# Optimization experiments

Hardware: AMD Instinct MI355X
Metric: run time of the kernel (lower is better)

Reference implementation:

```python
import jax, jax.numpy as jnp
from jax import lax
import numpy as np

EPS = 1e-3  # epsilon from __init__


def setup_inputs() -> dict:
    key = jax.random.key(0)
    k_x, k_m, k_v, k_p = jax.random.split(key, 4)
    B, C, H, W = 16, 64, 128, 128
    K = 8  # num_contexts
    x = jax.random.normal(k_x, (B, C, H, W), dtype=jnp.float32)
    # Parameters as initialized by reset_parameters():
    mean = jax.random.uniform(k_m, (K, 1), minval=-1.0, maxval=1.0, dtype=jnp.float32)
    variance = jax.random.uniform(k_v, (K, 1), minval=0.001, maxval=0.01, dtype=jnp.float32)
    p0 = jax.random.uniform(k_p, (K, 1), dtype=jnp.float32)
    prior = p0 / jnp.sum(p0, axis=0, keepdims=True)
    return {"x": x, "mean": mean, "variance": variance, "prior": prior}


def reference(x, mean, variance, prior):
    # Eval-mode forward of AdaptiveContextNorm (4D input path).
    mu = mean[:, 0]                      # (K,) scalar mean per context (expand over C is a broadcast)
    v = jax.nn.softplus(variance[:, 0])  # (K,)
    pr = jax.nn.softmax(prior[:, 0], axis=0)  # (K,)

    # Pass 1: mixture denominator. NOTE: faithful to source, the denominator
    # uses var WITHOUT +eps in the 4D path (ternary-precedence quirk), while
    # the numerator p_x_given_k uses (var + eps).
    def denom_step(acc, params):
        m, vv, pk = params
        return acc + pk * jnp.exp(-0.5 * ((x - m) / vv) ** 2), None

    denom, _ = lax.scan(denom_step, jnp.zeros_like(x), (mu, v, pr))

    # Pass 2: accumulate normalized output.
    def out_step(acc, params):
        m, vv, pk = params
        p_x_given_k = pk * jnp.exp(-0.5 * ((x - m) / (vv + EPS)) ** 2)
        tau_k = p_x_given_k / (denom + EPS)
        hat_x = (x - m) / jnp.sqrt(vv + EPS)
        return acc + tau_k / jnp.sqrt(pk + EPS) * hat_x, None

    out, _ = lax.scan(out_step, jnp.zeros_like(x), (mu, v, pr))
    return out
```

## Files before the change

kernel.cpp:

```cpp
#include <hip/hip_runtime.h>
#include <hip/hip_fp16.h>

#define ACN_EPS   0.001f
#define ACN_LOG2E 1.4426950408889634f
#define ACN_LN2   0.6931471805599453f
#define TBL_N     2048
#define TBL_LO    -8.0f
#define TBL_SCALE 128.0f
#define TBL_OFF   1024.0f
#define TBL_MAX_T 2047.999f

typedef float v4f  __attribute__((ext_vector_type(4)));
typedef unsigned int u32;
typedef u32 v4u __attribute__((ext_vector_type(4)));

__device__ __forceinline__ float acn_F_fast(float x, const float* mu,
                                            const float* s1, const float* lp,
                                            const float* s2, const float* lw) {
    float denom = 0.0f, S = 0.0f;
#pragma unroll
    for (int k = 0; k < 8; ++k) {
        float d  = x - mu[k];
        float d2 = d * d;
        denom += __builtin_amdgcn_exp2f(fmaf(s1[k], d2, lp[k]));
        S = fmaf(__builtin_amdgcn_exp2f(fmaf(s2[k], d2, lw[k])), d, S);
    }
    return S * __builtin_amdgcn_rcpf(denom + ACN_EPS);
}

__global__ void acn_build(const float* __restrict__ mean,
                          const float* __restrict__ variance,
                          const float* __restrict__ prior,
                          u32* __restrict__ T) {
    int i = blockIdx.x * blockDim.x + threadIdx.x;
    if (i >= TBL_N) return;

    float mu[8], s1[8], lp[8], s2[8], lw[8], e[8];
    float mx = -1e30f;
#pragma unroll
    for (int k = 0; k < 8; ++k) { e[k] = prior[k]; mx = fmaxf(mx, e[k]); }
    float sum = 0.0f;
#pragma unroll
    for (int k = 0; k < 8; ++k) {
        e[k] = __builtin_amdgcn_exp2f((e[k] - mx) * ACN_LOG2E);
        sum += e[k];
    }
    float rs = __builtin_amdgcn_rcpf(sum);
#pragma unroll
    for (int k = 0; k < 8; ++k) {
        float pk = e[k] * rs;
        float v  = __builtin_amdgcn_logf(1.0f +
                     __builtin_amdgcn_exp2f(variance[k] * ACN_LOG2E)) * ACN_LN2;
        float ve = v + ACN_EPS;
        float rv  = __builtin_amdgcn_rcpf(v);
        float rve = __builtin_amdgcn_rcpf(ve);
        mu[k] = mean[k];
        s1[k] = -0.5f * ACN_LOG2E * rv * rv;
        s2[k] = -0.5f * ACN_LOG2E * rve * rve;
        lp[k] = __builtin_amdgcn_logf(pk);
        lw[k] = lp[k] - 0.5f * __builtin_amdgcn_logf(pk + ACN_EPS)
                      - 0.5f * __builtin_amdgcn_logf(ve);
    }

    const float h  = 1.0f / TBL_SCALE;
    float x0 = TBL_LO + (float)i * h;
    float y0 = acn_F_fast(x0,     mu, s1, lp, s2, lw);
    float y1 = acn_F_fast(x0 + h, mu, s1, lp, s2, lw);
    __half2 hv = __halves2half2(__float2half(y0), __float2half(y1 - y0));
    T[i] = *(const u32*)&hv;
}

__device__ __forceinline__ float acn_interp(const u32* tbl, float xx) {
    float t  = fmaf(xx, TBL_SCALE, TBL_OFF);
    t        = __builtin_amdgcn_fmed3f(t, 0.0f, TBL_MAX_T);
    int   ii = (int)t;
    float f  = t - (float)ii;
    u32 u = tbl[ii];
    __half2 hv = *(const __half2*)&u;
    return fmaf(__high2float(hv), f, __low2float(hv));
}

__device__ __forceinline__ v4f acn_interp4(const u32* tbl, v4f xv) {
    v4f r;
    r.x = acn_interp(tbl, xv.x);
    r.y = acn_interp(tbl, xv.y);
    r.z = acn_interp(tbl, xv.z);
    r.w = acn_interp(tbl, xv.w);
    return r;
}

__global__ __launch_bounds__(256) void acn_main(const v4f* __restrict__ x,
                                                v4f* __restrict__ out,
                                                const v4u* __restrict__ T,
                                                int n4) {
    __shared__ u32 tbl[TBL_N];

    const int Tn  = gridDim.x * blockDim.x;
    const int idx = blockIdx.x * blockDim.x + threadIdx.x;

    if (n4 == 8 * Tn) {
        v4f a = x[idx];
        v4f b = x[idx + Tn];

        v4u t0 = T[threadIdx.x];
        v4u t1 = T[threadIdx.x + 256];
        *(v4u*)&tbl[threadIdx.x * 4]         = t0;
        *(v4u*)&tbl[(threadIdx.x + 256) * 4] = t1;
        __syncthreads();

#pragma unroll
        for (int c = 0; c < 4; ++c) {
            const int i = idx + c * 2 * Tn;
            v4f an, bn;
            if (c < 3) {
                an = x[i + 2 * Tn];
                bn = x[i + 3 * Tn];
            }
            __builtin_nontemporal_store(acn_interp4(tbl, a), &out[i]);
            __builtin_nontemporal_store(acn_interp4(tbl, b), &out[i + Tn]);
            if (c < 3) { a = an; b = bn; }
        }
    } else {
        for (int i = threadIdx.x; i < TBL_N / 4; i += 256)
            *(v4u*)&tbl[i * 4] = T[i];
        __syncthreads();
        for (int i = idx; i < n4; i += Tn) {
            __builtin_nontemporal_store(acn_interp4(tbl, x[i]), &out[i]);
        }
    }
}

extern "C" void kernel_launch(void* const* d_in, const int* in_sizes, int n_in,
                              void* d_out, int out_size, void* d_ws, size_t ws_size,
                              hipStream_t stream) {
    const float* x        = (const float*)d_in[0];
    const float* mean     = (const float*)d_in[1];
    const float* variance = (const float*)d_in[2];
    const float* prior    = (const float*)d_in[3];
    float* out = (float*)d_out;
    u32*   T   = (u32*)d_ws;

    acn_build<<<TBL_N / 256, 256, 0, stream>>>(mean, variance, prior, T);

    int n4 = out_size / 4;
    const int block = 256;
    const int grid  = 2048;
    acn_main<<<grid, block, 0, stream>>>((const v4f*)x, (v4f*)out,
                                         (const v4u*)T, n4);
}
```

Measured before the change: 114.6 us.

## Fuse lookup-table build into main kernel and halve grid size

Removes the separate table-build kernel. Each block now computes the 2048-entry half-precision interpolation table in shared memory itself, with every thread producing 8 consecutive entries from 9 evaluations of the mixture. The grid is halved to 1024 blocks, each handling 16 vectors per thread. Loading the first x values before the build is meant to overlap the table computation with global memory latency. This drops one kernel launch and the workspace round trip, but every block repeats the table arithmetic (about 144 exp2 per thread).

```diff
diff --git a/kernel.cpp b/kernel.cpp
--- a/kernel.cpp
+++ b/kernel.cpp
@@ -13,62 +13,6 @@
 typedef float v4f  __attribute__((ext_vector_type(4)));
 typedef unsigned int u32;
 typedef u32 v4u __attribute__((ext_vector_type(4)));
-
-__device__ __forceinline__ float acn_F_fast(float x, const float* mu,
-                                            const float* s1, const float* lp,
-                                            const float* s2, const float* lw) {
-    float denom = 0.0f, S = 0.0f;
-#pragma unroll
-    for (int k = 0; k < 8; ++k) {
-        float d  = x - mu[k];
-        float d2 = d * d;
-        denom += __builtin_amdgcn_exp2f(fmaf(s1[k], d2, lp[k]));
-        S = fmaf(__builtin_amdgcn_exp2f(fmaf(s2[k], d2, lw[k])), d, S);
-    }
-    return S * __builtin_amdgcn_rcpf(denom + ACN_EPS);
-}
-
-__global__ void acn_build(const float* __restrict__ mean,
-                          const float* __restrict__ variance,
-                          const float* __restrict__ prior,
-                          u32* __restrict__ T) {
-    int i = blockIdx.x * blockDim.x + threadIdx.x;
-    if (i >= TBL_N) return;
-
-    float mu[8], s1[8], lp[8], s2[8], lw[8], e[8];
-    float mx = -1e30f;
-#pragma unroll
-    for (int k = 0; k < 8; ++k) { e[k] = prior[k]; mx = fmaxf(mx, e[k]); }
-    float sum = 0.0f;
-#pragma unroll
-    for (int k = 0; k < 8; ++k) {
-        e[k] = __builtin_amdgcn_exp2f((e[k] - mx) * ACN_LOG2E);
-        sum += e[k];
-    }
-    float rs = __builtin_amdgcn_rcpf(sum);
-#pragma unroll
-    for (int k = 0; k < 8; ++k) {
-        float pk = e[k] * rs;
-        float v  = __builtin_amdgcn_logf(1.0f +
-                     __builtin_amdgcn_exp2f(variance[k] * ACN_LOG2E)) * ACN_LN2;
-        float ve = v + ACN_EPS;
-        float rv  = __builtin_amdgcn_rcpf(v);
-        float rve = __builtin_amdgcn_rcpf(ve);
-        mu[k] = mean[k];
-        s1[k] = -0.5f * ACN_LOG2E * rv * rv;
-        s2[k] = -0.5f * ACN_LOG2E * rve * rve;
-        lp[k] = __builtin_amdgcn_logf(pk);
-        lw[k] = lp[k] - 0.5f * __builtin_amdgcn_logf(pk + ACN_EPS)
-                      - 0.5f * __builtin_amdgcn_logf(ve);
-    }
-
-    const float h  = 1.0f / TBL_SCALE;
-    float x0 = TBL_LO + (float)i * h;
-    float y0 = acn_F_fast(x0,     mu, s1, lp, s2, lw);
-    float y1 = acn_F_fast(x0 + h, mu, s1, lp, s2, lw);
-    __half2 hv = __halves2half2(__float2half(y0), __float2half(y1 - y0));
-    T[i] = *(const u32*)&hv;
-}
 
 __device__ __forceinline__ float acn_interp(const u32* tbl, float xx) {
     float t  = fmaf(xx, TBL_SCALE, TBL_OFF);
@@ -89,41 +33,94 @@
     return r;
 }
 
-__global__ __launch_bounds__(256) void acn_main(const v4f* __restrict__ x,
-                                                v4f* __restrict__ out,
-                                                const v4u* __restrict__ T,
-                                                int n4) {
+__global__ __launch_bounds__(256, 4) void acn_fused(
+        const v4f* __restrict__ x,
+        v4f* __restrict__ out,
+        const float* __restrict__ mean,
+        const float* __restrict__ variance,
+        const float* __restrict__ prior,
+        int n4) {
     __shared__ u32 tbl[TBL_N];
 
     const int Tn  = gridDim.x * blockDim.x;
     const int idx = blockIdx.x * blockDim.x + threadIdx.x;
+    const bool fast = (n4 == 16 * Tn);
 
-    if (n4 == 8 * Tn) {
-        v4f a = x[idx];
-        v4f b = x[idx + Tn];
+    v4f a, b;
+    if (fast) { a = x[idx]; b = x[idx + Tn]; }
 
-        v4u t0 = T[threadIdx.x];
-        v4u t1 = T[threadIdx.x + 256];
-        *(v4u*)&tbl[threadIdx.x * 4]         = t0;
-        *(v4u*)&tbl[(threadIdx.x + 256) * 4] = t1;
-        __syncthreads();
+    {
+        float e[8];
+        float mx = -1e30f;
+#pragma unroll
+        for (int k = 0; k < 8; ++k) { e[k] = prior[k]; mx = fmaxf(mx, e[k]); }
+        float sum = 0.0f;
+#pragma unroll
+        for (int k = 0; k < 8; ++k) {
+            e[k] = __builtin_amdgcn_exp2f((e[k] - mx) * ACN_LOG2E);
+            sum += e[k];
+        }
+        float rs = __builtin_amdgcn_rcpf(sum);
+
+        const float h  = 1.0f / TBL_SCALE;
+        const float x0 = TBL_LO + (float)(threadIdx.x * 8) * h;
+
+        float denom[9], S[9];
+#pragma unroll
+        for (int j = 0; j < 9; ++j) { denom[j] = 0.0f; S[j] = 0.0f; }
 
 #pragma unroll
-        for (int c = 0; c < 4; ++c) {
+        for (int k = 0; k < 8; ++k) {
+            float pk = e[k] * rs;
+            float v  = __builtin_amdgcn_logf(1.0f +
+                         __builtin_amdgcn_exp2f(variance[k] * ACN_LOG2E)) * ACN_LN2;
+            float ve = v + ACN_EPS;
+            float rv  = __builtin_amdgcn_rcpf(v);
+            float rve = __builtin_amdgcn_rcpf(ve);
+            float mu  = mean[k];
+            float s1  = -0.5f * ACN_LOG2E * rv * rv;
+            float s2  = -0.5f * ACN_LOG2E * rve * rve;
+            float lp  = __builtin_amdgcn_logf(pk);
+            float lw  = lp - 0.5f * __builtin_amdgcn_logf(pk + ACN_EPS)
+                           - 0.5f * __builtin_amdgcn_logf(ve);
+#pragma unroll
+            for (int j = 0; j < 9; ++j) {
+                float d  = x0 + (float)j * h - mu;
+                float d2 = d * d;
+                denom[j] += __builtin_amdgcn_exp2f(fmaf(s1, d2, lp));
+                S[j] = fmaf(__builtin_amdgcn_exp2f(fmaf(s2, d2, lw)), d, S[j]);
+            }
+        }
+
+        u32 packed[8];
+        float y_prev = S[0] * __builtin_amdgcn_rcpf(denom[0] + ACN_EPS);
+#pragma unroll
+        for (int j = 0; j < 8; ++j) {
+            float y_next = S[j + 1] * __builtin_amdgcn_rcpf(denom[j + 1] + ACN_EPS);
+            __half2 hv = __halves2half2(__float2half(y_prev),
+                                        __float2half(y_next - y_prev));
+            packed[j] = *(const u32*)&hv;
+            y_prev = y_next;
+        }
+        *(v4u*)&tbl[threadIdx.x * 8]     = *(v4u*)&packed[0];
+        *(v4u*)&tbl[threadIdx.x * 8 + 4] = *(v4u*)&packed[4];
+    }
+    __syncthreads();
+
+    if (fast) {
+#pragma unroll
+        for (int c = 0; c < 8; ++c) {
             const int i = idx + c * 2 * Tn;
             v4f an, bn;
-            if (c < 3) {
+            if (c < 7) {
                 an = x[i + 2 * Tn];
                 bn = x[i + 3 * Tn];
             }
             __builtin_nontemporal_store(acn_interp4(tbl, a), &out[i]);
             __builtin_nontemporal_store(acn_interp4(tbl, b), &out[i + Tn]);
-            if (c < 3) { a = an; b = bn; }
+            if (c < 7) { a = an; b = bn; }
         }
     } else {
-        for (int i = threadIdx.x; i < TBL_N / 4; i += 256)
-            *(v4u*)&tbl[i * 4] = T[i];
-        __syncthreads();
         for (int i = idx; i < n4; i += Tn) {
             __builtin_nontemporal_store(acn_interp4(tbl, x[i]), &out[i]);
         }
@@ -138,13 +135,11 @@
     const float* variance = (const float*)d_in[2];
     const float* prior    = (const float*)d_in[3];
     float* out = (float*)d_out;
-    u32*   T   = (u32*)d_ws;
-
-    acn_build<<<TBL_N / 256, 256, 0, stream>>>(mean, variance, prior, T);
+    (void)d_ws; (void)ws_size;
 
     int n4 = out_size / 4;
     const int block = 256;
-    const int grid  = 2048;
-    acn_main<<<grid, block, 0, stream>>>((const v4f*)x, (v4f*)out,
-                                         (const v4u*)T, n4);
+    const int grid  = 1024;
+    acn_fused<<<grid, block, 0, stream>>>((const v4f*)x, (v4f*)out,
+                                          mean, variance, prior, n4);
 }
```

After: 114.6 us. No clear change (+0.0%).
